# Optimization experiments

Measured on AMD Instinct MI355X. Metric: run time of the kernel, lower is better.

Reference implementation:

```python
import jax, jax.numpy as jnp
import numpy as np

NUM_ITER = 10
DIM = 512
SPATIAL = 28 * 28  # 784


def sqrt_newton_schulz(A, num_iter=NUM_ITER):
    # A: [B, D, D] SPD-ish bilinear matrix
    B, D = A.shape[0], A.shape[1]
    norm_A = jnp.sqrt(jnp.sum(A * A, axis=(1, 2)))  # Frobenius norm, [B]
    norm_A3 = norm_A[:, None, None]
    Y = A / norm_A3
    I = jnp.broadcast_to(jnp.eye(D, dtype=A.dtype), (B, D, D))
    Z = I
    for _ in range(num_iter):
        T = 0.5 * (3.0 * I - jnp.matmul(Z, Y))
        Y = jnp.matmul(Y, T)
        Z = jnp.matmul(T, Z)
    return Y * jnp.sqrt(norm_A)[:, None, None]


def setup_inputs() -> dict:
    key = jax.random.key(0)
    k1, k2 = jax.random.split(key)
    X = jax.random.normal(k1, (64, DIM, 28, 28), dtype=jnp.float32)
    fc_weight = jax.random.normal(k2, (200, DIM * DIM), dtype=jnp.float32) * 0.01
    fc_bias = jnp.zeros((200,), dtype=jnp.float32)
    return {"X": X, "fc_weight": fc_weight, "fc_bias": fc_bias}


def reference(X, fc_weight, fc_bias):
    B = X.shape[0]
    x = X.reshape(B, DIM, SPATIAL)                      # [B, 512, 784]
    A = jnp.einsum('bip,bjp->bij', x, x) / SPATIAL      # bilinear pooling [B,512,512]
    Y = sqrt_newton_schulz(A, NUM_ITER)                 # matrix square root
    v = Y.reshape(B, DIM * DIM)
    v = jnp.sign(v) * jnp.sqrt(jnp.abs(v) + 1e-5)       # signed sqrt
    n = jnp.sqrt(jnp.sum(v * v, axis=1, keepdims=True))
    v = v / jnp.maximum(n, 1e-12)                       # L2 normalize (F.normalize)
    return v @ fc_weight.T + fc_bias                    # [B, 200]
```

## Files before the change

kernel.cpp:

```cpp
#include <hip/hip_runtime.h>
#include <math.h>
#include <stdint.h>

#define DIMM 512
#define SLOT_S 262144

typedef __attribute__((ext_vector_type(8))) _Float16 half8v;
typedef __attribute__((ext_vector_type(8))) unsigned short ushort8v;
typedef __attribute__((ext_vector_type(4))) float f32x4;

__device__ __forceinline__ unsigned short f2h(float f) {
    _Float16 h = (_Float16)f;
    return __builtin_bit_cast(unsigned short, h);
}
__device__ __forceinline__ float h2f(unsigned short u) {
    return (float)__builtin_bit_cast(_Float16, u);
}
__device__ __forceinline__ float sgn_sqrt(float tv)
{
    float r = sqrtf(fabsf(tv) + 1e-5f);
    return tv > 0.f ? r : (tv < 0.f ? -r : 0.f);
}

__global__ __launch_bounds__(256) void ns_single(
    const unsigned short* __restrict__ A0, const unsigned short* __restrict__ A1,
    const unsigned short* __restrict__ Bb,
    unsigned short* __restrict__ C0, unsigned short* __restrict__ C1,
    int lda, long aslot, int ldb, long bslot, int K,
    int mode, const float* __restrict__ norm, int nz)
{
    __shared__ __align__(16) unsigned short sm[8960];

    const int nwg = gridDim.x;
    const int chunk = nwg >> 3;
    const int bid = blockIdx.x;
    const int wu = (bid & 7) * chunk + (bid >> 3);
    const int per_batch = nz * 10;
    const int bz = wu / per_batch;
    const int rr = wu - bz * per_batch;
    const int z  = rr / 10;
    const int tile = rr - z * 10;
    int ti, tj;
    if (tile < 4)      { ti = 0; tj = tile; }
    else if (tile < 7) { ti = 1; tj = tile - 3; }
    else if (tile < 9) { ti = 2; tj = tile - 5; }
    else               { ti = 3; tj = 3; }

    const unsigned short* A  = (z ? A1 : A0) + (size_t)bz * aslot;
    const unsigned short* Bp = Bb + (size_t)bz * bslot;
    unsigned short* C = (z ? C1 : C0) + (size_t)bz * SLOT_S;

    float rn = 1.0f, sq = 0.0f;
    if (mode != 0) {
        const float nv = norm[bz];
        rn = 1.0f / nv;
        sq = sqrtf(nv);
    }
    const _Float16 bscale = (_Float16)((mode == 1 || mode == 2) ? (-0.5f * rn) : -0.5f);
    const float csc = (mode == 1) ? rn : 1.0f;

    const int m0 = ti * 128;
    const int n0 = tj * 128;

    const int t = threadIdx.x;
    const int l = t & 63;
    const int w = t >> 6;
    const int wr = w >> 1, wc = w & 1;
    const int lr = l & 15;
    const int sc = (((l >> 4) ^ ((l >> 1) & 3)) << 3);

    const int sr = t >> 1, sh = t & 1;
    const int swz = (sr >> 1) & 3;
    const int slot0 = ((((sh << 1) | 0) ^ swz) << 3);
    const int slot1 = ((((sh << 1) | 1) ^ swz) << 3);
    const int wbase = sr * 32;
    const unsigned short* pA = A  + (size_t)(m0 + sr) * lda + sh * 16;
    const unsigned short* pB = Bp + (size_t)(n0 + sr) * ldb + sh * 16;
    const int dbase = (n0 + sr) - sh * 16;

    f32x4 acc[4][4] = {};

    ushort8v a0, a1, b0, b1;
#define LOADALL(OFF) do { \
    a0 = *(const ushort8v*)(pA + (OFF));  a1 = *(const ushort8v*)(pA + (OFF) + 8); \
    b0 = *(const ushort8v*)(pB + (OFF));  b1 = *(const ushort8v*)(pB + (OFF) + 8); \
  } while (0)

#define CONVB(S) do { \
    half8v bv0 = __builtin_bit_cast(half8v, b0); \
    half8v bv1 = __builtin_bit_cast(half8v, b1); \
    bv0 *= bscale; bv1 *= bscale; \
    const int dj = dbase - (S) * 32; \
    _Pragma("unroll") \
    for (int j = 0; j < 8; ++j) { \
        if (dj == j)     bv0[j] += (_Float16)1.5f; \
        if (dj == j + 8) bv1[j] += (_Float16)1.5f; \
    } \
    b0 = __builtin_bit_cast(ushort8v, bv0); \
    b1 = __builtin_bit_cast(ushort8v, bv1); \
  } while (0)

    LOADALL(0);
    CONVB(0);
    const int nsteps = K >> 5;
    for (int s = 0; s < nsteps; ++s) {
        __syncthreads();
        *(ushort8v*)&sm[       wbase + slot0] = a0; *(ushort8v*)&sm[       wbase + slot1] = a1;
        *(ushort8v*)&sm[4096 + wbase + slot0] = b0; *(ushort8v*)&sm[4096 + wbase + slot1] = b1;
        __syncthreads();
        if (s + 1 < nsteps) { LOADALL((s + 1) * 32); CONVB(s + 1); }

        half8v ah[4], bh[4];
#pragma unroll
        for (int f = 0; f < 4; ++f) {
            const int ra = ((wr * 64 + f * 16 + lr) << 5) + sc;
            const int rb = ((wc * 64 + f * 16 + lr) << 5) + sc;
            ah[f] = *(const half8v*)(&sm[ra]);
            bh[f] = *(const half8v*)(&sm[4096 + rb]);
        }
#pragma unroll
        for (int fm = 0; fm < 4; ++fm)
#pragma unroll
            for (int fn = 0; fn < 4; ++fn)
                acc[fm][fn] = __builtin_amdgcn_mfma_f32_16x16x32_f16(ah[fm], bh[fn], acc[fm][fn], 0, 0, 0);
    }
#undef LOADALL
#undef CONVB

#pragma unroll
    for (int fm = 0; fm < 4; ++fm) {
#pragma unroll
        for (int j = 0; j < 4; ++j) {
            const int row = m0 + wr * 64 + fm * 16 + (l >> 4) * 4 + j;
            const size_t crow = (size_t)row * 512;
#pragma unroll
            for (int fn = 0; fn < 4; ++fn) {
                const int col = n0 + wc * 64 + fn * 16 + lr;
                float v = csc * acc[fm][fn][j];
                if (mode == 3) v = sgn_sqrt(v * sq);
                acc[fm][fn][j] = v;
                C[crow + col] = f2h(v);
            }
        }
    }

    if (ti != tj) {
        const int TP = 70;
        unsigned short* smT = sm;
        const int cst = wc * 64 + lr;
        const int r4  = (l >> 4) * 4;
        const int rc2 = t >> 1;
        const int chh = t & 1;
        __syncthreads();
#pragma unroll
        for (int h = 0; h < 2; ++h) {
            if (wr == h) {
#pragma unroll
                for (int fm = 0; fm < 4; ++fm) {
#pragma unroll
                    for (int fn = 0; fn < 4; ++fn) {
                        ushort4 q;
                        q.x = f2h(acc[fm][fn][0]);
                        q.y = f2h(acc[fm][fn][1]);
                        q.z = f2h(acc[fm][fn][2]);
                        q.w = f2h(acc[fm][fn][3]);
                        *(ushort4*)&smT[(cst + fn * 16) * TP + r4 + fm * 16] = q;
                    }
                }
            }
            __syncthreads();
            {
                unsigned short* dst = C + (size_t)(n0 + rc2) * 512 + m0 + h * 64 + chh * 32;
                const unsigned short* srcp = &smT[rc2 * TP + chh * 32];
#pragma unroll
                for (int k = 0; k < 8; ++k)
                    *(ushort4*)(dst + k * 4) = *(const ushort4*)(srcp + k * 4);
            }
            __syncthreads();
        }
    }
}

__global__ __launch_bounds__(256) void gram_single(const float* __restrict__ X,
                                                   unsigned short* __restrict__ C0,
                                                   float alpha, int K)
{
    __shared__ __align__(16) unsigned short sm[8960];

    const int nwg = gridDim.x;
    const int chunk = nwg >> 3;
    const int wu = (blockIdx.x & 7) * chunk + (blockIdx.x >> 3);
    const int bz = wu / 10, tile = wu - bz * 10;
    int ti, tj;
    if (tile < 4)      { ti = 0; tj = tile; }
    else if (tile < 7) { ti = 1; tj = tile - 3; }
    else if (tile < 9) { ti = 2; tj = tile - 5; }
    else               { ti = 3; tj = 3; }
    const int m0 = ti * 128, n0 = tj * 128;
    unsigned short* C = C0 + (size_t)bz * SLOT_S;

    const int t = threadIdx.x;
    const int l = t & 63;
    const int w = t >> 6;
    const int wr = w >> 1, wc = w & 1;
    const int lr = l & 15;
    const int sc = (((l >> 4) ^ ((l >> 1) & 3)) << 3);

    const int sr = t >> 1, sh = t & 1;
    const int swz = (sr >> 1) & 3;
    const int slot0 = ((((sh << 1) | 0) ^ swz) << 3);
    const int slot1 = ((((sh << 1) | 1) ^ swz) << 3);
    const int wbase = sr * 32;

    const float* pXa = X + ((size_t)bz * 512 + m0 + sr) * 784 + sh * 16;
    const float* pXb = X + ((size_t)bz * 512 + n0 + sr) * 784 + sh * 16;

    f32x4 acc[4][4] = {};

    float4 xa0, xa1, xa2, xa3, xb0, xb1, xb2, xb3;
    ushort8v a0, a1, b0, b1;

#define GLD(OFF) do { \
    if ((OFF) + sh * 16 < 784) { \
        xa0 = *(const float4*)(pXa + (OFF));      xa1 = *(const float4*)(pXa + (OFF) + 4); \
        xa2 = *(const float4*)(pXa + (OFF) + 8);  xa3 = *(const float4*)(pXa + (OFF) + 12); \
        xb0 = *(const float4*)(pXb + (OFF));      xb1 = *(const float4*)(pXb + (OFF) + 4); \
        xb2 = *(const float4*)(pXb + (OFF) + 8);  xb3 = *(const float4*)(pXb + (OFF) + 12); \
    } else { \
        xa0 = xa1 = xa2 = xa3 = make_float4(0.f, 0.f, 0.f, 0.f); \
        xb0 = xb1 = xb2 = xb3 = make_float4(0.f, 0.f, 0.f, 0.f); \
    } } while (0)

#define CV8(F0, F1, O) do { \
    (O)[0] = f2h((F0).x); (O)[1] = f2h((F0).y); \
    (O)[2] = f2h((F0).z); (O)[3] = f2h((F0).w); \
    (O)[4] = f2h((F1).x); (O)[5] = f2h((F1).y); \
    (O)[6] = f2h((F1).z); (O)[7] = f2h((F1).w); \
  } while (0)

#define CONVALL() do { \
    CV8(xa0, xa1, a0); CV8(xa2, xa3, a1); \
    CV8(xb0, xb1, b0); CV8(xb2, xb3, b1); \
  } while (0)

    GLD(0);
    CONVALL();
    const int nsteps = K >> 5;
    for (int s = 0; s < nsteps; ++s) {
        __syncthreads();
        *(ushort8v*)&sm[       wbase + slot0] = a0; *(ushort8v*)&sm[       wbase + slot1] = a1;
        *(ushort8v*)&sm[4096 + wbase + slot0] = b0; *(ushort8v*)&sm[4096 + wbase + slot1] = b1;
        __syncthreads();
        if (s + 1 < nsteps) GLD((s + 1) * 32);

        half8v ah[4], bh[4];
#pragma unroll
        for (int f = 0; f < 4; ++f) {
            const int ra = ((wr * 64 + f * 16 + lr) << 5) + sc;
            const int rb = ((wc * 64 + f * 16 + lr) << 5) + sc;
            ah[f] = *(const half8v*)(&sm[ra]);
            bh[f] = *(const half8v*)(&sm[4096 + rb]);
        }
#pragma unroll
        for (int fm = 0; fm < 4; ++fm)
#pragma unroll
            for (int fn = 0; fn < 4; ++fn)
                acc[fm][fn] = __builtin_amdgcn_mfma_f32_16x16x32_f16(ah[fm], bh[fn], acc[fm][fn], 0, 0, 0);
        if (s + 1 < nsteps) CONVALL();
    }
#undef GLD
#undef CV8
#undef CONVALL

#pragma unroll
    for (int fm = 0; fm < 4; ++fm) {
#pragma unroll
        for (int j = 0; j < 4; ++j) {
            const int row = m0 + wr * 64 + fm * 16 + (l >> 4) * 4 + j;
            const size_t crow = (size_t)row * 512;
#pragma unroll
            for (int fn = 0; fn < 4; ++fn) {
                const int col = n0 + wc * 64 + fn * 16 + lr;
                float v = acc[fm][fn][j] * alpha;
                acc[fm][fn][j] = v;
                C[crow + col] = f2h(v);
            }
        }
    }

    if (ti != tj) {
        const int TP = 70;
        unsigned short* smT = sm;
        const int cst = wc * 64 + lr;
        const int r4  = (l >> 4) * 4;
        const int rc2 = t >> 1;
        const int chh = t & 1;
        __syncthreads();
#pragma unroll
        for (int h = 0; h < 2; ++h) {
            if (wr == h) {
#pragma unroll
                for (int fm = 0; fm < 4; ++fm) {
#pragma unroll
                    for (int fn = 0; fn < 4; ++fn) {
                        ushort4 q;
                        q.x = f2h(acc[fm][fn][0]);
                        q.y = f2h(acc[fm][fn][1]);
                        q.z = f2h(acc[fm][fn][2]);
                        q.w = f2h(acc[fm][fn][3]);
                        *(ushort4*)&smT[(cst + fn * 16) * TP + r4 + fm * 16] = q;
                    }
                }
            }
            __syncthreads();
            {
                unsigned short* dst = C + (size_t)(n0 + rc2) * 512 + m0 + h * 64 + chh * 32;
                const unsigned short* srcp = &smT[rc2 * TP + chh * 32];
#pragma unroll
                for (int k = 0; k < 8; ++k)
                    *(ushort4*)(dst + k * 4) = *(const ushort4*)(srcp + k * 4);
            }
            __syncthreads();
        }
    }
}

__global__ __launch_bounds__(256) void frob_s(const unsigned short* __restrict__ P,
                                              float* __restrict__ pp)
{
    const int b = blockIdx.x >> 3, sg = blockIdx.x & 7;
    const unsigned short* p = P + (size_t)b * SLOT_S + sg * 32768;
    float s = 0.f;
    for (int i = threadIdx.x * 8; i < 32768; i += 2048) {
        ushort8v h = *(const ushort8v*)(p + i);
#pragma unroll
        for (int j = 0; j < 8; ++j) {
            float v = h2f(h[j]);
            s += v * v;
        }
    }
    __shared__ float red[256];
    red[threadIdx.x] = s;
    __syncthreads();
    for (int wd = 128; wd > 0; wd >>= 1) {
        if (threadIdx.x < wd) red[threadIdx.x] += red[threadIdx.x + wd];
        __syncthreads();
    }
    if (threadIdx.x == 0) pp[blockIdx.x] = red[0];
}

__global__ __launch_bounds__(64) void frob_fin(const float* __restrict__ pp,
                                               float* __restrict__ out)
{
    const int b = threadIdx.x;
    float s = 0.f;
#pragma unroll
    for (int i = 0; i < 8; ++i) s += pp[b * 8 + i];
    out[b] = sqrtf(s);
}

__global__ __launch_bounds__(256) void fc_mfma_s(
    const unsigned short* __restrict__ Vp, const float* __restrict__ Wfc,
    float* __restrict__ part)
{
    __shared__ __align__(16) unsigned short sm2[6144];

    const int sp = blockIdx.x >> 1;
    const int nt = blockIdx.x & 1;
    const int kbase = sp * 2048;
    const int n0 = nt * 128;

    const int t = threadIdx.x;
    const int l = t & 63;
    const int w = t >> 6;
    const int wr = w >> 1, wc = w & 1;
    const int lr = l & 15;
    const int sc = (((l >> 4) ^ ((l >> 1) & 3)) << 3);

    const int sr = t >> 1, sh = t & 1;
    const int swz = (sr >> 1) & 3;
    const int slot0 = ((((sh << 1) | 0) ^ swz) << 3);
    const int slot1 = ((((sh << 1) | 1) ^ swz) << 3);

    const unsigned short* gA = Vp + (size_t)sr * SLOT_S + kbase + sh * 16;
    const int wrow = n0 + sr;
    const bool wv = wrow < 200;
    const float* gB = Wfc + (size_t)wrow * 262144 + kbase + sh * 16;

    f32x4 acc[2][4] = {};

    ushort8v va0, va1, vb0, vb1;
    float4 wf0, wf1, wf2, wf3;
#define FLOAD(OFF) do { \
    if (t < 128) { \
        va0 = *(const ushort8v*)(gA + (OFF)); va1 = *(const ushort8v*)(gA + (OFF) + 8); \
    } \
    if (wv) { \
        wf0 = *(const float4*)(gB + (OFF));      wf1 = *(const float4*)(gB + (OFF) + 4); \
        wf2 = *(const float4*)(gB + (OFF) + 8);  wf3 = *(const float4*)(gB + (OFF) + 12); \
    } else { \
        wf0 = wf1 = wf2 = wf3 = make_float4(0.f, 0.f, 0.f, 0.f); \
    } \
    vb0[0] = f2h(wf0.x); vb0[1] = f2h(wf0.y); vb0[2] = f2h(wf0.z); vb0[3] = f2h(wf0.w); \
    vb0[4] = f2h(wf1.x); vb0[5] = f2h(wf1.y); vb0[6] = f2h(wf1.z); vb0[7] = f2h(wf1.w); \
    vb1[0] = f2h(wf2.x); vb1[1] = f2h(wf2.y); vb1[2] = f2h(wf2.z); vb1[3] = f2h(wf2.w); \
    vb1[4] = f2h(wf3.x); vb1[5] = f2h(wf3.y); vb1[6] = f2h(wf3.z); vb1[7] = f2h(wf3.w); \
  } while (0)

    FLOAD(0);
    for (int s = 0; s < 64; ++s) {
        __syncthreads();
        if (t < 128) {
            *(ushort8v*)&sm2[(sr << 5) + slot0] = va0;
            *(ushort8v*)&sm2[(sr << 5) + slot1] = va1;
        }
        *(ushort8v*)&sm2[2048 + (sr << 5) + slot0] = vb0;
        *(ushort8v*)&sm2[2048 + (sr << 5) + slot1] = vb1;
        __syncthreads();
        if (s + 1 < 64) FLOAD((s + 1) * 32);

        half8v ah[2], bh[4];
#pragma unroll
        for (int f = 0; f < 2; ++f) {
            const int ra = ((wr * 32 + f * 16 + lr) << 5) + sc;
            ah[f] = *(const half8v*)(&sm2[ra]);
        }
#pragma unroll
        for (int f = 0; f < 4; ++f) {
            const int rb = ((wc * 64 + f * 16 + lr) << 5) + sc;
            bh[f] = *(const half8v*)(&sm2[2048 + rb]);
        }
#pragma unroll
        for (int fm = 0; fm < 2; ++fm)
#pragma unroll
            for (int fn = 0; fn < 4; ++fn)
                acc[fm][fn] = __builtin_amdgcn_mfma_f32_16x16x32_f16(ah[fm], bh[fn], acc[fm][fn], 0, 0, 0);
    }
#undef FLOAD

    float* pb = part + (size_t)(sp * 2 + nt) * 64 * 128;
#pragma unroll
    for (int fm = 0; fm < 2; ++fm)
#pragma unroll
        for (int j = 0; j < 4; ++j) {
            const int row = wr * 32 + fm * 16 + (l >> 4) * 4 + j;
#pragma unroll
            for (int fn = 0; fn < 4; ++fn) {
                const int col = wc * 64 + fn * 16 + lr;
                pb[(size_t)row * 128 + col] = acc[fm][fn][j];
            }
        }
}

__global__ __launch_bounds__(256) void fc_reduce(
    const float* __restrict__ part, const float* __restrict__ n2,
    const float* __restrict__ bias, float* __restrict__ out)
{
    const int p = blockIdx.x * 256 + threadIdx.x;
    if (p >= 64 * 200) return;
    const int b = p / 200, o = p % 200;
    const int nt = o >> 7, n = o & 127;
    float s = 0.f;
    for (int c = 0; c < 128; ++c)
        s += part[((size_t)(c * 2 + nt) * 64 + b) * 128 + n];
    const float nb = fmaxf(n2[b], 1e-12f);
    out[p] = s / nb + bias[o];
}

extern "C" void kernel_launch(void* const* d_in, const int* in_sizes, int n_in,
                              void* d_out, int out_size, void* d_ws, size_t ws_size,
                              hipStream_t stream)
{
    const float* X    = (const float*)d_in[0];
    const float* Wfc  = (const float*)d_in[1];
    const float* bias = (const float*)d_in[2];
    float* out = (float*)d_out;

    float* norm  = (float*)d_ws;
    float* norm2 = norm + 64;
    float* fpart = norm2 + 64;
    float* part  = fpart + 512;
    unsigned short* region = (unsigned short*)(part + (size_t)256 * 64 * 128);

    unsigned short* P[4];
    for (int i = 0; i < 4; ++i) P[i] = region + (size_t)i * 64 * SLOT_S;

    gram_single<<<640, 256, 0, stream>>>(X, P[0], 1.0f / 784.0f, 800);
    frob_s<<<512, 256, 0, stream>>>(P[0], fpart);
    frob_fin<<<1, 64, 0, stream>>>(fpart, norm);

    ns_single<<<640, 256, 0, stream>>>(P[0], P[0], P[0], P[2], P[2],
        512, (long)SLOT_S, 512, (long)SLOT_S, 512, 1, norm, 1);
    ns_single<<<640, 256, 0, stream>>>(P[2], P[2], P[0], P[3], P[3],
        512, (long)SLOT_S, 512, (long)SLOT_S, 512, 2, norm, 1);

    unsigned short *Y = P[2], *M = P[3], *F0 = P[0], *F1 = P[1];
    for (int it = 1; it <= 8; ++it) {
        ns_single<<<1280, 256, 0, stream>>>(M, Y, M, F0, F1,
            512, (long)SLOT_S, 512, (long)SLOT_S, 512, 0, norm, 2);
        ns_single<<<640, 256, 0, stream>>>(F0, F0, M, Y, Y,
            512, (long)SLOT_S, 512, (long)SLOT_S, 512, 0, norm, 1);
        unsigned short* Mold = M;
        M = Y;
        Y = F1;
        F1 = Mold;
    }
    ns_single<<<640, 256, 0, stream>>>(Y, Y, M, F0, F0,
        512, (long)SLOT_S, 512, (long)SLOT_S, 512, 3, norm, 1);

    unsigned short* Vp = F0;
    frob_s<<<512, 256, 0, stream>>>(Vp, fpart);
    frob_fin<<<1, 64, 0, stream>>>(fpart, norm2);
    fc_mfma_s<<<dim3(256), 256, 0, stream>>>(Vp, Wfc, part);
    fc_reduce<<<50, 256, 0, stream>>>(part, norm2, bias, out);
}
```

Baseline: 994.1 us.

## Move 1.5I-0.5X transform to epilogue and double K-step to 64

The per-step B-operand conversion (scaling by -0.5 and adding 1.5 on the diagonal) is removed from the main loop. The affine form is now applied in the epilogue as 1.5*A - 0.5*scale*acc, which needs an extra global read of A per output element. The K tile grows from 32 to 64 with a wider XOR swizzle and more shared memory, halving the number of barriers per GEMM. The cost is more registers and LDS per block, which may reduce occupancy.

```diff
diff --git a/kernel.cpp b/kernel.cpp
--- a/kernel.cpp
+++ b/kernel.cpp
@@ -29,7 +29,7 @@
     int lda, long aslot, int ldb, long bslot, int K,
     int mode, const float* __restrict__ norm, int nz)
 {
-    __shared__ __align__(16) unsigned short sm[8960];
+    __shared__ __align__(16) unsigned short sm[16384];
 
     const int nwg = gridDim.x;
     const int chunk = nwg >> 3;
@@ -56,8 +56,7 @@
         rn = 1.0f / nv;
         sq = sqrtf(nv);
     }
-    const _Float16 bscale = (_Float16)((mode == 1 || mode == 2) ? (-0.5f * rn) : -0.5f);
-    const float csc = (mode == 1) ? rn : 1.0f;
+    const float kscale = (mode == 1 || mode == 2) ? rn : 1.0f;
 
     const int m0 = ti * 128;
     const int n0 = tj * 128;
@@ -67,77 +66,72 @@
     const int w = t >> 6;
     const int wr = w >> 1, wc = w & 1;
     const int lr = l & 15;
-    const int sc = (((l >> 4) ^ ((l >> 1) & 3)) << 3);
+    const int rs0 = (((l >> 4) + 0) ^ (lr & 7)) << 3;
+    const int rs1 = (((l >> 4) + 4) ^ (lr & 7)) << 3;
 
     const int sr = t >> 1, sh = t & 1;
-    const int swz = (sr >> 1) & 3;
-    const int slot0 = ((((sh << 1) | 0) ^ swz) << 3);
-    const int slot1 = ((((sh << 1) | 1) ^ swz) << 3);
-    const int wbase = sr * 32;
-    const unsigned short* pA = A  + (size_t)(m0 + sr) * lda + sh * 16;
-    const unsigned short* pB = Bp + (size_t)(n0 + sr) * ldb + sh * 16;
-    const int dbase = (n0 + sr) - sh * 16;
+    const int ws0 = (((sh << 2) | 0) ^ (sr & 7)) << 3;
+    const int ws1 = (((sh << 2) | 1) ^ (sr & 7)) << 3;
+    const int ws2 = (((sh << 2) | 2) ^ (sr & 7)) << 3;
+    const int ws3 = (((sh << 2) | 3) ^ (sr & 7)) << 3;
+    const int wbase = sr << 6;
+    const unsigned short* pA = A  + (size_t)(m0 + sr) * lda + sh * 32;
+    const unsigned short* pB = Bp + (size_t)(n0 + sr) * ldb + sh * 32;
 
     f32x4 acc[4][4] = {};
 
-    ushort8v a0, a1, b0, b1;
+    ushort8v a0, a1, a2, a3, b0, b1, b2, b3;
 #define LOADALL(OFF) do { \
-    a0 = *(const ushort8v*)(pA + (OFF));  a1 = *(const ushort8v*)(pA + (OFF) + 8); \
-    b0 = *(const ushort8v*)(pB + (OFF));  b1 = *(const ushort8v*)(pB + (OFF) + 8); \
+    a0 = *(const ushort8v*)(pA + (OFF));       a1 = *(const ushort8v*)(pA + (OFF) + 8); \
+    a2 = *(const ushort8v*)(pA + (OFF) + 16);  a3 = *(const ushort8v*)(pA + (OFF) + 24); \
+    b0 = *(const ushort8v*)(pB + (OFF));       b1 = *(const ushort8v*)(pB + (OFF) + 8); \
+    b2 = *(const ushort8v*)(pB + (OFF) + 16);  b3 = *(const ushort8v*)(pB + (OFF) + 24); \
   } while (0)
 
-#define CONVB(S) do { \
-    half8v bv0 = __builtin_bit_cast(half8v, b0); \
-    half8v bv1 = __builtin_bit_cast(half8v, b1); \
-    bv0 *= bscale; bv1 *= bscale; \
-    const int dj = dbase - (S) * 32; \
-    _Pragma("unroll") \
-    for (int j = 0; j < 8; ++j) { \
-        if (dj == j)     bv0[j] += (_Float16)1.5f; \
-        if (dj == j + 8) bv1[j] += (_Float16)1.5f; \
-    } \
-    b0 = __builtin_bit_cast(ushort8v, bv0); \
-    b1 = __builtin_bit_cast(ushort8v, bv1); \
-  } while (0)
-
     LOADALL(0);
-    CONVB(0);
-    const int nsteps = K >> 5;
+    const int nsteps = K >> 6;
     for (int s = 0; s < nsteps; ++s) {
         __syncthreads();
-        *(ushort8v*)&sm[       wbase + slot0] = a0; *(ushort8v*)&sm[       wbase + slot1] = a1;
-        *(ushort8v*)&sm[4096 + wbase + slot0] = b0; *(ushort8v*)&sm[4096 + wbase + slot1] = b1;
-        __syncthreads();
-        if (s + 1 < nsteps) { LOADALL((s + 1) * 32); CONVB(s + 1); }
-
-        half8v ah[4], bh[4];
-#pragma unroll
-        for (int f = 0; f < 4; ++f) {
-            const int ra = ((wr * 64 + f * 16 + lr) << 5) + sc;
-            const int rb = ((wc * 64 + f * 16 + lr) << 5) + sc;
-            ah[f] = *(const half8v*)(&sm[ra]);
-            bh[f] = *(const half8v*)(&sm[4096 + rb]);
-        }
-#pragma unroll
-        for (int fm = 0; fm < 4; ++fm)
-#pragma unroll
-            for (int fn = 0; fn < 4; ++fn)
-                acc[fm][fn] = __builtin_amdgcn_mfma_f32_16x16x32_f16(ah[fm], bh[fn], acc[fm][fn], 0, 0, 0);
+        *(ushort8v*)&sm[       wbase + ws0] = a0; *(ushort8v*)&sm[       wbase + ws1] = a1;
+        *(ushort8v*)&sm[       wbase + ws2] = a2; *(ushort8v*)&sm[       wbase + ws3] = a3;
+        *(ushort8v*)&sm[8192 + wbase + ws0] = b0; *(ushort8v*)&sm[8192 + wbase + ws1] = b1;
+        *(ushort8v*)&sm[8192 + wbase + ws2] = b2; *(ushort8v*)&sm[8192 + wbase + ws3] = b3;
+        __syncthreads();
+        if (s + 1 < nsteps) LOADALL((s + 1) * 64);
+
+#pragma unroll
+        for (int ks = 0; ks < 2; ++ks) {
+            const int rsl = ks ? rs1 : rs0;
+            half8v ah[4], bh[4];
+#pragma unroll
+            for (int f = 0; f < 4; ++f) {
+                const int ra = ((wr * 64 + f * 16 + lr) << 6) + rsl;
+                const int rb = ((wc * 64 + f * 16 + lr) << 6) + rsl;
+                ah[f] = *(const half8v*)(&sm[ra]);
+                bh[f] = *(const half8v*)(&sm[8192 + rb]);
+            }
+#pragma unroll
+            for (int fm = 0; fm < 4; ++fm)
+#pragma unroll
+                for (int fn = 0; fn < 4; ++fn)
+                    acc[fm][fn] = __builtin_amdgcn_mfma_f32_16x16x32_f16(ah[fm], bh[fn], acc[fm][fn], 0, 0, 0);
+        }
     }
 #undef LOADALL
-#undef CONVB
 
 #pragma unroll
     for (int fm = 0; fm < 4; ++fm) {
 #pragma unroll
         for (int j = 0; j < 4; ++j) {
             const int row = m0 + wr * 64 + fm * 16 + (l >> 4) * 4 + j;
+            const unsigned short* arow = A + (size_t)row * lda;
             const size_t crow = (size_t)row * 512;
 #pragma unroll
             for (int fn = 0; fn < 4; ++fn) {
                 const int col = n0 + wc * 64 + fn * 16 + lr;
-                float v = csc * acc[fm][fn][j];
-                if (mode == 3) v = sgn_sqrt(v * sq);
+                float v = 1.5f * h2f(arow[col]) - 0.5f * kscale * acc[fm][fn][j];
+                if (mode == 1) v *= rn;
+                else if (mode == 3) v = sgn_sqrt(v * sq);
                 acc[fm][fn][j] = v;
                 C[crow + col] = f2h(v);
             }
```

Result: slower. 1.304 ms (+31.2%).
